# Performance work log

Measured on AMD Instinct MI355X. Metric: run time of the kernel, lower is better.

The kernel has to match this reference:

```python
import jax, jax.numpy as jnp
import numpy as np

N = 100000   # num nodes
E = 500000   # num hyperedges
NNZ = 1600000
H, C = 4, 32
IN_CH = 128


def setup_inputs() -> dict:
    key = jax.random.key(0)
    k1, k2, k3, k4, k5 = jax.random.split(key, 5)
    X = jax.random.normal(k1, (N, IN_CH), dtype=jnp.float32)
    W = jax.random.normal(k2, (IN_CH, H * C), dtype=jnp.float32) * (1.0 / np.sqrt(IN_CH))
    att_e = jax.random.normal(k3, (1, H, C), dtype=jnp.float32) * 0.1
    vertex = jax.random.randint(k4, (NNZ,), 0, N, dtype=jnp.int64)
    edges = jax.random.randint(k5, (NNZ,), 0, E, dtype=jnp.int64)
    return {"X": X, "W": W, "att_e": att_e, "vertex": vertex, "edges": edges}


def reference(X, W, att_e, vertex, edges):
    n = X.shape[0]
    X0 = X @ W                                  # [N, H*C]
    Xh = X0.reshape(n, H, C)                    # [N, H, C]
    Xve = Xh[vertex]                            # [nnz, H, C] gather
    # scatter-mean over hyperedges
    esum = jax.ops.segment_sum(Xve, edges, num_segments=E)            # [E, H, C]
    cnt = jax.ops.segment_sum(jnp.ones((Xve.shape[0],), X.dtype), edges, num_segments=E)
    Xe = esum / jnp.maximum(cnt, 1.0)[:, None, None]                  # [E, H, C]
    # per-edge attention score
    alpha_e = (Xe * att_e).sum(-1)              # [E, H]
    a_ev = alpha_e[edges]                       # [nnz, H]
    alpha = jax.nn.leaky_relu(a_ev, 0.01)
    # segment softmax over vertex groups
    m = jax.ops.segment_max(alpha, vertex, num_segments=n)            # [N, H]
    ex = jnp.exp(alpha - m[vertex])
    den = jax.ops.segment_sum(ex, vertex, num_segments=n)             # [N, H]
    alpha = ex / (den[vertex] + 1e-16)          # [nnz, H]
    # weighted scatter-sum back to nodes
    Xev = Xe[edges] * alpha[:, :, None]         # [nnz, H, C]
    Xv = jax.ops.segment_sum(Xev, vertex, num_segments=n)             # [N, H, C]
    return Xv.reshape(n, H * C) + X0
```

## Files before the change

### kernel.cpp

```cpp
#include <hip/hip_runtime.h>
#include <hip/hip_bf16.h>
#include <hip/hip_fp16.h>
#include <cstdint>

#define NH 4
#define HC 128
#define INCH 128
#define NEDGE 500000
#define NN 100000

#define KE_SHIFT 11
#define KV_SHIFT 9
#define KE (1 << KE_SHIFT)
#define KV (1 << KV_SHIFT)
#define NBE 245
#define NBV 196
#define CAP_E 8192
#define CAP_V 10240
#define CHUNK_A 4096

typedef float          f32x2 __attribute__((ext_vector_type(2)));
typedef float          f32x4 __attribute__((ext_vector_type(4)));
typedef float          f32x8 __attribute__((ext_vector_type(8)));
typedef unsigned int   u32x2 __attribute__((ext_vector_type(2)));
typedef unsigned short u16x8 __attribute__((ext_vector_type(8)));

static __device__ __forceinline__ unsigned short f2bf(float f){
  union { float f; unsigned u; } v; v.f = f;
  unsigned r = v.u + 0x7fffu + ((v.u >> 16) & 1u);
  return (unsigned short)(r >> 16);
}
static __device__ __forceinline__ float bf2f(unsigned short b){
  union { unsigned u; float f; } v; v.u = ((unsigned)b) << 16;
  return v.f;
}
static __device__ __forceinline__ f32x8 bf8f(u16x8 b){
  f32x8 r;
  r[0]=bf2f(b[0]); r[1]=bf2f(b[1]); r[2]=bf2f(b[2]); r[3]=bf2f(b[3]);
  r[4]=bf2f(b[4]); r[5]=bf2f(b[5]); r[6]=bf2f(b[6]); r[7]=bf2f(b[7]);
  return r;
}

#if __has_builtin(__builtin_amdgcn_cvt_pk_fp8_f32) && __has_builtin(__builtin_amdgcn_cvt_pk_f32_fp8)
#define FP8_HW 1
#else
#define FP8_HW 0
#endif

#if !FP8_HW
static __device__ __forceinline__ unsigned enc1_fp8(float v){
  union{ __half h; unsigned short u; } c; c.h = __float2half(v);
  unsigned u = c.u;
  unsigned s = (u>>15)&1u, e=(u>>10)&31u, m=u&0x3FFu;
  int e8 = (int)e - 8;
  unsigned lsb = (m>>7)&1u;
  unsigned m8 = (m + 63u + lsb) >> 7;
  if (m8 == 8u){ m8 = 0u; e8 += 1; }
  if (e8 <= 0)  return s<<7;
  if (e8 >= 16) return (s<<7)|0x7Eu;
  return (s<<7)|((unsigned)e8<<3)|m8;
}
static __device__ __forceinline__ float dec1_fp8(unsigned b){
  unsigned s=(b>>7)&1u, e=(b>>3)&15u, m=b&7u;
  union{unsigned u; float f;} r;
  if (e==0u){ r.f = (float)m * 0.001953125f; if(s) r.f = -r.f; }
  else r.u = (s<<31)|((e+120u)<<23)|(m<<20);
  return r.f;
}
#endif

static __device__ __forceinline__ u32x2 pack8_fp8(const f32x8 v){
  u32x2 w;
#if FP8_HW
  int w0 = __builtin_amdgcn_cvt_pk_fp8_f32(v[0], v[1], 0, false);
  w0     = __builtin_amdgcn_cvt_pk_fp8_f32(v[2], v[3], w0, true);
  int w1 = __builtin_amdgcn_cvt_pk_fp8_f32(v[4], v[5], 0, false);
  w1     = __builtin_amdgcn_cvt_pk_fp8_f32(v[6], v[7], w1, true);
  w.x = (unsigned)w0; w.y = (unsigned)w1;
#else
  w.x = enc1_fp8(v[0]) | (enc1_fp8(v[1])<<8) | (enc1_fp8(v[2])<<16) | (enc1_fp8(v[3])<<24);
  w.y = enc1_fp8(v[4]) | (enc1_fp8(v[5])<<8) | (enc1_fp8(v[6])<<16) | (enc1_fp8(v[7])<<24);
#endif
  return w;
}
static __device__ __forceinline__ void fma8s_fp8(f32x8& acc, float c, float w, u32x2 q){
#if FP8_HW
  f32x2 p;
  p = __builtin_amdgcn_cvt_pk_f32_fp8((int)q.x, false); acc[0]=acc[0]*c + w*p.x; acc[1]=acc[1]*c + w*p.y;
  p = __builtin_amdgcn_cvt_pk_f32_fp8((int)q.x, true ); acc[2]=acc[2]*c + w*p.x; acc[3]=acc[3]*c + w*p.y;
  p = __builtin_amdgcn_cvt_pk_f32_fp8((int)q.y, false); acc[4]=acc[4]*c + w*p.x; acc[5]=acc[5]*c + w*p.y;
  p = __builtin_amdgcn_cvt_pk_f32_fp8((int)q.y, true ); acc[6]=acc[6]*c + w*p.x; acc[7]=acc[7]*c + w*p.y;
#else
  acc[0]=acc[0]*c + w*dec1_fp8(q.x&0xFF);        acc[1]=acc[1]*c + w*dec1_fp8((q.x>>8)&0xFF);
  acc[2]=acc[2]*c + w*dec1_fp8((q.x>>16)&0xFF);  acc[3]=acc[3]*c + w*dec1_fp8(q.x>>24);
  acc[4]=acc[4]*c + w*dec1_fp8(q.y&0xFF);        acc[5]=acc[5]*c + w*dec1_fp8((q.y>>8)&0xFF);
  acc[6]=acc[6]*c + w*dec1_fp8((q.y>>16)&0xFF);  acc[7]=acc[7]*c + w*dec1_fp8(q.y>>24);
#endif
}

#define GBM 128
#define GBK 16
__global__ __launch_bounds__(256) void gemmA_fused(const float* __restrict__ X,
                                                   const float* __restrict__ Wm,
                                                   const float* __restrict__ att,
                                                   unsigned short* __restrict__ X0bf,
                                                   float* __restrict__ score, int nrows,
                                                   const int* __restrict__ vertex,
                                                   const int* __restrict__ edges, int nnz,
                                                   int* __restrict__ cursE, int* __restrict__ cursV,
                                                   unsigned* __restrict__ stgE, unsigned* __restrict__ stgV,
                                                   int nA){
  __shared__ float As[GBK][GBM+4];
  __shared__ float Bs[GBK][HC+4];
  __shared__ float sc[GBM][17];
  __shared__ int cE[NBE], c2E[NBE], gE[NBE];
  __shared__ int cV[NBV], c2V[NBV], gV[NBV];
  const int t = threadIdx.x;

  if ((int)blockIdx.x < nA){
    const int base = blockIdx.x * CHUNK_A;
    int ev[16], vv[16];
    #pragma unroll
    for (int j=0;j<16;j++){
      int i = base + t + j*256;
      if (i < nnz){ ev[j] = edges[i]; vv[j] = vertex[i]; }
      else ev[j] = -1;
    }
    for (int j=t;j<NBE;j+=256){ cE[j]=0; c2E[j]=0; }
    for (int j=t;j<NBV;j+=256){ cV[j]=0; c2V[j]=0; }
    __syncthreads();
    #pragma unroll
    for (int j=0;j<16;j++) if (ev[j]>=0){
      atomicAdd(&cE[ev[j]>>KE_SHIFT], 1);
      atomicAdd(&cV[vv[j]>>KV_SHIFT], 1);
    }
    __syncthreads();
    for (int j=t;j<NBE;j+=256) gE[j] = atomicAdd(&cursE[j], cE[j]);
    for (int j=t;j<NBV;j+=256) gV[j] = atomicAdd(&cursV[j], cV[j]);
    __syncthreads();
    #pragma unroll
    for (int j=0;j<16;j++) if (ev[j]>=0){
      int bE = ev[j]>>KE_SHIFT;
      int p = gE[bE] + atomicAdd(&c2E[bE],1);
      if (p < CAP_E) stgE[(size_t)bE*CAP_E + p] = ((unsigned)vv[j] << KE_SHIFT) | (unsigned)(ev[j] & (KE-1));
      int bV = vv[j]>>KV_SHIFT;
      int q = gV[bV] + atomicAdd(&c2V[bV],1);
      if (q < CAP_V) stgV[(size_t)bV*CAP_V + q] = ((unsigned)ev[j] << KV_SHIFT) | (unsigned)(vv[j] & (KV-1));
    }
    return;
  }

  const int row0 = (blockIdx.x - nA) * GBM;
  const int trow = t >> 4;
  const int tcol = t & 15;
  float acc[8][8];
  #pragma unroll
  for (int i=0;i<8;i++)
    #pragma unroll
    for (int j=0;j<8;j++) acc[i][j]=0.f;

  for (int k0=0;k0<INCH;k0+=GBK){
    #pragma unroll
    for (int l = t; l < 512; l += 256){
      int r  = l >> 2;
      int ks = (l & 3) * 4;
      int grow = row0 + r;
      float4 v = make_float4(0.f,0.f,0.f,0.f);
      if (grow < nrows) v = *(const float4*)(X + (size_t)grow*INCH + k0 + ks);
      As[ks+0][r]=v.x; As[ks+1][r]=v.y; As[ks+2][r]=v.z; As[ks+3][r]=v.w;
    }
    #pragma unroll
    for (int l = t; l < 512; l += 256){
      int r  = l >> 5;
      int cs = (l & 31) * 4;
      float4 v = *(const float4*)(Wm + (size_t)(k0+r)*HC + cs);
      *(float4*)(&Bs[r][cs]) = v;
    }
    __syncthreads();
    #pragma unroll
    for (int kk=0;kk<GBK;kk++){
      float a[8], b[8];
      *(float4*)&a[0] = *(float4*)&As[kk][trow*8];
      *(float4*)&a[4] = *(float4*)&As[kk][trow*8+4];
      *(float4*)&b[0] = *(float4*)&Bs[kk][tcol*8];
      *(float4*)&b[4] = *(float4*)&Bs[kk][tcol*8+4];
      #pragma unroll
      for (int i=0;i<8;i++)
        #pragma unroll
        for (int j=0;j<8;j++) acc[i][j] = fmaf(a[i], b[j], acc[i][j]);
    }
    __syncthreads();
  }
  float attv[8];
  *(float4*)&attv[0] = *(const float4*)(att + tcol*8);
  *(float4*)&attv[4] = *(const float4*)(att + tcol*8 + 4);
  #pragma unroll
  for (int i=0;i<8;i++){
    int grow = row0 + trow*8 + i;
    float p = 0.f;
    #pragma unroll
    for (int j=0;j<8;j++) p = fmaf(acc[i][j], attv[j], p);
    sc[trow*8+i][tcol] = p;
    if (grow < nrows){
      ushort4 b0, b1;
      b0.x=f2bf(acc[i][0]); b0.y=f2bf(acc[i][1]); b0.z=f2bf(acc[i][2]); b0.w=f2bf(acc[i][3]);
      b1.x=f2bf(acc[i][4]); b1.y=f2bf(acc[i][5]); b1.z=f2bf(acc[i][6]); b1.w=f2bf(acc[i][7]);
      *(ushort4*)(X0bf + (size_t)grow*HC + tcol*8    ) = b0;
      *(ushort4*)(X0bf + (size_t)grow*HC + tcol*8 + 4) = b1;
    }
  }
  __syncthreads();
  for (int idx = t; idx < GBM*NH; idx += 256){
    int row = idx >> 2, h = idx & 3;
    int grow = row0 + row;
    if (grow < nrows){
      float s = sc[row][4*h] + sc[row][4*h+1] + sc[row][4*h+2] + sc[row][4*h+3];
      score[(size_t)grow*NH + h] = s;
    }
  }
}

template<int K, int CAP, int IT, int SHIFT, int NB>
__device__ __forceinline__ void phaseB_body(const unsigned* __restrict__ stg,
                                            const int* __restrict__ curs,
                                            int* __restrict__ offsOut,
                                            int* __restrict__ csrOut, int nKeys, int b,
                                            int* cur, int* tsum, int* bsh){
  const int t = threadIdx.x;
  const int k0 = b * K;
  const int kc = min(K, nKeys - k0);
  int c = (t < NB) ? min(curs[t], CAP) : 0;
  bsh[t] = c; __syncthreads();
  for (int d2=1; d2<512; d2<<=1){
    int x = (t>=d2) ? bsh[t-d2] : 0; __syncthreads();
    bsh[t] += x; __syncthreads();
  }
  const int gbase = (b > 0) ? bsh[b-1] : 0;
  const int cnt   = min(curs[b], CAP);
  if (b == NB-1 && t == 0) offsOut[nKeys] = bsh[NB-1];
  unsigned it[IT];
  #pragma unroll
  for (int j=0;j<IT;j++){
    int i = t + j*512;
    it[j] = (i < cnt) ? stg[(size_t)b*CAP + i] : 0xFFFFFFFFu;
  }
  for (int j=t;j<K;j+=512) cur[j] = 0;
  __syncthreads();
  #pragma unroll
  for (int j=0;j<IT;j++) if (it[j] != 0xFFFFFFFFu) atomicAdd(&cur[it[j] & (K-1)], 1);
  __syncthreads();
  constexpr int KPT = K / 512;
  int loc[KPT]; int s = 0;
  #pragma unroll
  for (int j=0;j<KPT;j++){ loc[j] = s; s += cur[t*KPT + j]; }
  tsum[t] = s; __syncthreads();
  for (int d2=1; d2<512; d2<<=1){
    int x = (t>=d2) ? tsum[t-d2] : 0; __syncthreads();
    tsum[t] += x; __syncthreads();
  }
  const int tbase = tsum[t] - s;
  __syncthreads();
  #pragma unroll
  for (int j=0;j<KPT;j++){
    int k = t*KPT + j;
    int abs0 = gbase + tbase + loc[j];
    if (k < kc) offsOut[k0 + k] = abs0;
    cur[k] = abs0;
  }
  __syncthreads();
  #pragma unroll
  for (int j=0;j<IT;j++) if (it[j] != 0xFFFFFFFFu){
    int pos = atomicAdd(&cur[it[j] & (K-1)], 1);
    csrOut[pos] = (int)(it[j] >> SHIFT);
  }
}

__global__ __launch_bounds__(512) void phaseB_fused(const unsigned* __restrict__ stgE,
                                                    const unsigned* __restrict__ stgV,
                                                    const int* __restrict__ cursE,
                                                    const int* __restrict__ cursV,
                                                    int* __restrict__ eoffs, int* __restrict__ voffs,
                                                    int* __restrict__ ecsr, int* __restrict__ vcsr){
  __shared__ int cur[KE];
  __shared__ int tsum[512];
  __shared__ int bsh[512];
  const int b = blockIdx.x;
  if (b < NBE) phaseB_body<KE, CAP_E, CAP_E/512, KE_SHIFT, NBE>(stgE, cursE, eoffs, ecsr, NEDGE, b, cur, tsum, bsh);
  else         phaseB_body<KV, CAP_V, CAP_V/512, KV_SHIFT, NBV>(stgV, cursV, voffs, vcsr, NN, b - NBE, cur, tsum, bsh);
}

__global__ __launch_bounds__(256) void edge_agg(const unsigned short* __restrict__ X0bf,
                                                const float* __restrict__ score,
                                                const int* __restrict__ ecsr,
                                                const int* __restrict__ eoffs,
                                                unsigned char* __restrict__ Xe8,
                                                float* __restrict__ alphaS, int E){
  int eg = blockIdx.x * 16 + (threadIdx.x >> 4);
  if (eg >= E) return;
  const int lane  = threadIdx.x & 15;
  const int cbase = lane * 8;
  const int start = eoffs[eg];
  const int d     = eoffs[eg+1] - start;
  f32x8 acc0 = {0.f,0.f,0.f,0.f,0.f,0.f,0.f,0.f};
  f32x8 acc1 = {0.f,0.f,0.f,0.f,0.f,0.f,0.f,0.f};
  float sacc0 = 0.f, sacc1 = 0.f;
  int k = 0;
  for (; k+1<d; k+=2){
    int v0 = ecsr[start + k];
    int v1 = ecsr[start + k + 1];
    u16x8 x0 = *(const u16x8*)(X0bf + (size_t)v0*HC + cbase);
    u16x8 x1 = *(const u16x8*)(X0bf + (size_t)v1*HC + cbase);
    if (lane < NH){
      sacc0 += score[(size_t)v0*NH + lane];
      sacc1 += score[(size_t)v1*NH + lane];
    }
    acc0 += bf8f(x0);
    acc1 += bf8f(x1);
  }
  if (k < d){
    int v0 = ecsr[start + k];
    u16x8 x0 = *(const u16x8*)(X0bf + (size_t)v0*HC + cbase);
    if (lane < NH) sacc0 += score[(size_t)v0*NH + lane];
    acc0 += bf8f(x0);
  }
  acc0 += acc1;
  const float inv = 1.0f / fmaxf((float)d, 1.0f);
  acc0 *= inv;
  float lm = fmaxf(fmaxf(fmaxf(fabsf(acc0[0]),fabsf(acc0[1])),fmaxf(fabsf(acc0[2]),fabsf(acc0[3]))),
                   fmaxf(fmaxf(fabsf(acc0[4]),fabsf(acc0[5])),fmaxf(fabsf(acc0[6]),fabsf(acc0[7]))));
  #pragma unroll
  for (int s=1; s<16; s<<=1) lm = fmaxf(lm, __shfl_xor(lm, s, 16));
  const float qs  = (lm > 1e-30f) ? 448.0f/lm : 0.f;
  const float dqs = (lm > 1e-30f) ? lm*(1.0f/448.0f) : 0.f;
  f32x8 q = acc0 * qs;
  u32x2 w = pack8_fp8(q);
  *(u32x2*)(Xe8 + (size_t)eg*HC + cbase) = w;
  if (lane < NH){
    float a = (sacc0 + sacc1) * inv;
    a = a > 0.f ? a : 0.01f*a;
    f32x2 rec = { a, dqs };
    *(f32x2*)(alphaS + (size_t)eg*8 + lane*2) = rec;
  }
}

__global__ __launch_bounds__(256) void vert_pass(const unsigned short* __restrict__ X0bf,
                                                 const unsigned char* __restrict__ Xe8,
                                                 const float* __restrict__ alphaS,
                                                 const int* __restrict__ vcsr,
                                                 const int* __restrict__ voffs,
                                                 float* __restrict__ out, int N){
  int n = blockIdx.x * 16 + (threadIdx.x >> 4);
  if (n >= N) return;
  const int lane  = threadIdx.x & 15;
  const int cbase = lane * 8;
  const int h2    = (lane >> 2) * 2;
  const size_t obase = (size_t)n*HC + cbase;
  f32x8 x0 = bf8f(*(const u16x8*)(X0bf + obase));
  const int start = voffs[n];
  const int d     = voffs[n+1] - start;
  if (d == 0){
    f32x4 lo = {x0[0],x0[1],x0[2],x0[3]}, hi = {x0[4],x0[5],x0[6],x0[7]};
    __builtin_nontemporal_store(lo, (f32x4*)(out + obase));
    __builtin_nontemporal_store(hi, (f32x4*)(out + obase + 4));
    return;
  }

  float m0=-1e30f, m1=-1e30f, m2=-1e30f, m3=-1e30f;
  float den0=0.f, den1=0.f, den2=0.f, den3=0.f;
  f32x8 acc0 = {0.f,0.f,0.f,0.f,0.f,0.f,0.f,0.f};
  f32x8 acc1 = {0.f,0.f,0.f,0.f,0.f,0.f,0.f,0.f};
  f32x8 acc2 = {0.f,0.f,0.f,0.f,0.f,0.f,0.f,0.f};
  f32x8 acc3 = {0.f,0.f,0.f,0.f,0.f,0.f,0.f,0.f};

#define UPD(i, ar, q) { \
    float mn_ = fmaxf(m##i, (ar).x); \
    float c_  = __expf(m##i - mn_); \
    float p_  = __expf((ar).x - mn_); \
    den##i = den##i * c_ + p_; \
    fma8s_fp8(acc##i, c_, p_ * (ar).y, (q)); \
    m##i = mn_; }

  int k = 0;
  for (; k+3<d; k+=4){
    int e0 = vcsr[start + k];
    int e1 = vcsr[start + k + 1];
    int e2 = vcsr[start + k + 2];
    int e3 = vcsr[start + k + 3];
    f32x2 ar0 = *(const f32x2*)(alphaS + (size_t)e0*8 + h2);
    f32x2 ar1 = *(const f32x2*)(alphaS + (size_t)e1*8 + h2);
    f32x2 ar2 = *(const f32x2*)(alphaS + (size_t)e2*8 + h2);
    f32x2 ar3 = *(const f32x2*)(alphaS + (size_t)e3*8 + h2);
    u32x2 q0 = *(const u32x2*)(Xe8 + (size_t)e0*HC + cbase);
    u32x2 q1 = *(const u32x2*)(Xe8 + (size_t)e1*HC + cbase);
    u32x2 q2 = *(const u32x2*)(Xe8 + (size_t)e2*HC + cbase);
    u32x2 q3 = *(const u32x2*)(Xe8 + (size_t)e3*HC + cbase);
    UPD(0, ar0, q0);
    UPD(1, ar1, q1);
    UPD(2, ar2, q2);
    UPD(3, ar3, q3);
  }
  for (; k<d; k++){
    int e0 = vcsr[start + k];
    f32x2 ar0 = *(const f32x2*)(alphaS + (size_t)e0*8 + h2);
    u32x2 q0 = *(const u32x2*)(Xe8 + (size_t)e0*HC + cbase);
    UPD(0, ar0, q0);
  }
#undef UPD

  float mn = fmaxf(fmaxf(m0,m1), fmaxf(m2,m3));
  float c0 = __expf(m0-mn), c1 = __expf(m1-mn), c2 = __expf(m2-mn), c3 = __expf(m3-mn);
  float den = den0*c0 + den1*c1 + den2*c2 + den3*c3;
  f32x8 acc = acc0*c0 + acc1*c1 + acc2*c2 + acc3*c3;
  const float w = 1.0f / (den + 1e-16f);
  acc = acc*w + x0;
  f32x4 lo = {acc[0],acc[1],acc[2],acc[3]};
  f32x4 hi = {acc[4],acc[5],acc[6],acc[7]};
  __builtin_nontemporal_store(lo, (f32x4*)(out + obase));
  __builtin_nontemporal_store(hi, (f32x4*)(out + obase + 4));
}

extern "C" void kernel_launch(void* const* d_in, const int* in_sizes, int n_in,
                              void* d_out, int out_size, void* d_ws, size_t ws_size,
                              hipStream_t stream){
  const float* X   = (const float*)d_in[0];
  const float* Wm  = (const float*)d_in[1];
  const float* att = (const float*)d_in[2];
  const int* vertex = (const int*)d_in[3];
  const int* edges  = (const int*)d_in[4];
  const int N   = in_sizes[0] / INCH;
  const int NNZ = in_sizes[3];
  const int E   = NEDGE;

  char* ws = (char*)d_ws;
  size_t off = 0;
  auto alloc = [&](size_t bytes)->char*{
    char* p = ws + off;
    off += (bytes + 255) & ~(size_t)255;
    return p;
  };
  unsigned char*  Xe8    = (unsigned char*)alloc((size_t)E * HC);
  unsigned short* X0bf   = (unsigned short*)alloc((size_t)NN * HC * sizeof(unsigned short));
  float*          score  = (float*)alloc((size_t)NN * NH * sizeof(float));
  float*          alphaS = (float*)alloc((size_t)E * 8 * sizeof(float));
  int*            eoffs  = (int*)alloc((size_t)(E+1) * sizeof(int));
  int*            voffs  = (int*)alloc((size_t)(NN+1) * sizeof(int));
  int*            ecsr   = (int*)alloc((size_t)NNZ * sizeof(int));
  int*            vcsr   = (int*)alloc((size_t)NNZ * sizeof(int));
  int*            curs   = (int*)alloc((size_t)(NBE + NBV) * sizeof(int));
  int*            cursE  = curs;
  int*            cursV  = curs + NBE;
  unsigned* stgE = (unsigned*)(void*)Xe8;
  unsigned* stgV = (unsigned*)((char*)(void*)Xe8 + (size_t)NBE * CAP_E * sizeof(unsigned));

  const int nGemm = (N + GBM - 1) / GBM;
  const int nA    = (NNZ + CHUNK_A - 1) / CHUNK_A;

  hipMemsetAsync(curs, 0, (size_t)(NBE + NBV) * sizeof(int), stream);
  gemmA_fused<<<nA + nGemm, 256, 0, stream>>>(X, Wm, att, X0bf, score, N,
                                              vertex, edges, NNZ, cursE, cursV, stgE, stgV, nA);
  phaseB_fused<<<NBE + NBV, 512, 0, stream>>>(stgE, stgV, cursE, cursV, eoffs, voffs, ecsr, vcsr);
  edge_agg<<<(E + 15)/16, 256, 0, stream>>>(X0bf, score, ecsr, eoffs, Xe8, alphaS, E);
  vert_pass<<<(N + 15)/16, 256, 0, stream>>>(X0bf, Xe8, alphaS, vcsr, voffs, (float*)d_out, N);
}
```

Before: 256.8 us.

## Split fused GEMM/binning kernel, enlarge binning blocks, pack alpha records as fp16

Separates the combined GEMM and COO-binning kernel into two launches. Binning now runs in 512-thread blocks over 8192-element chunks, which halves the number of global cursor atomics. The per-edge alpha record shrinks from eight floats to a 16-byte record: four fp16 leaky-relu scores plus the fp32 dequant scale. vert_pass now issues one 16-byte load per edge instead of a strided f32x2 gather. The costs are an extra kernel launch, lost overlap between the GEMM and binning, and fp16 precision on the attention scores.

```diff
diff --git a/kernel.cpp b/kernel.cpp
--- a/kernel.cpp
+++ b/kernel.cpp
@@ -17,12 +17,13 @@
 #define NBV 196
 #define CAP_E 8192
 #define CAP_V 10240
-#define CHUNK_A 4096
+#define CHUNK_A 8192
 
 typedef float          f32x2 __attribute__((ext_vector_type(2)));
 typedef float          f32x4 __attribute__((ext_vector_type(4)));
 typedef float          f32x8 __attribute__((ext_vector_type(8)));
 typedef unsigned int   u32x2 __attribute__((ext_vector_type(2)));
+typedef unsigned int   u32x4 __attribute__((ext_vector_type(4)));
 typedef unsigned short u16x8 __attribute__((ext_vector_type(8)));
 
 static __device__ __forceinline__ unsigned short f2bf(float f){
@@ -100,59 +101,18 @@
 
 #define GBM 128
 #define GBK 16
-__global__ __launch_bounds__(256) void gemmA_fused(const float* __restrict__ X,
-                                                   const float* __restrict__ Wm,
-                                                   const float* __restrict__ att,
-                                                   unsigned short* __restrict__ X0bf,
-                                                   float* __restrict__ score, int nrows,
-                                                   const int* __restrict__ vertex,
-                                                   const int* __restrict__ edges, int nnz,
-                                                   int* __restrict__ cursE, int* __restrict__ cursV,
-                                                   unsigned* __restrict__ stgE, unsigned* __restrict__ stgV,
-                                                   int nA){
+__global__ __launch_bounds__(256) void gemm_x0(const float* __restrict__ X,
+                                               const float* __restrict__ Wm,
+                                               const float* __restrict__ att,
+                                               unsigned short* __restrict__ X0bf,
+                                               float* __restrict__ score, int nrows){
   __shared__ float As[GBK][GBM+4];
   __shared__ float Bs[GBK][HC+4];
   __shared__ float sc[GBM][17];
-  __shared__ int cE[NBE], c2E[NBE], gE[NBE];
-  __shared__ int cV[NBV], c2V[NBV], gV[NBV];
-  const int t = threadIdx.x;
-
-  if ((int)blockIdx.x < nA){
-    const int base = blockIdx.x * CHUNK_A;
-    int ev[16], vv[16];
-    #pragma unroll
-    for (int j=0;j<16;j++){
-      int i = base + t + j*256;
-      if (i < nnz){ ev[j] = edges[i]; vv[j] = vertex[i]; }
-      else ev[j] = -1;
-    }
-    for (int j=t;j<NBE;j+=256){ cE[j]=0; c2E[j]=0; }
-    for (int j=t;j<NBV;j+=256){ cV[j]=0; c2V[j]=0; }
-    __syncthreads();
-    #pragma unroll
-    for (int j=0;j<16;j++) if (ev[j]>=0){
-      atomicAdd(&cE[ev[j]>>KE_SHIFT], 1);
-      atomicAdd(&cV[vv[j]>>KV_SHIFT], 1);
-    }
-    __syncthreads();
-    for (int j=t;j<NBE;j+=256) gE[j] = atomicAdd(&cursE[j], cE[j]);
-    for (int j=t;j<NBV;j+=256) gV[j] = atomicAdd(&cursV[j], cV[j]);
-    __syncthreads();
-    #pragma unroll
-    for (int j=0;j<16;j++) if (ev[j]>=0){
-      int bE = ev[j]>>KE_SHIFT;
-      int p = gE[bE] + atomicAdd(&c2E[bE],1);
-      if (p < CAP_E) stgE[(size_t)bE*CAP_E + p] = ((unsigned)vv[j] << KE_SHIFT) | (unsigned)(ev[j] & (KE-1));
-      int bV = vv[j]>>KV_SHIFT;
-      int q = gV[bV] + atomicAdd(&c2V[bV],1);
-      if (q < CAP_V) stgV[(size_t)bV*CAP_V + q] = ((unsigned)ev[j] << KV_SHIFT) | (unsigned)(vv[j] & (KV-1));
-    }
-    return;
-  }
-
-  const int row0 = (blockIdx.x - nA) * GBM;
-  const int trow = t >> 4;
-  const int tcol = t & 15;
+  const int tid  = threadIdx.x;
+  const int row0 = blockIdx.x * GBM;
+  const int trow = tid >> 4;
+  const int tcol = tid & 15;
   float acc[8][8];
   #pragma unroll
   for (int i=0;i<8;i++)
@@ -161,7 +121,7 @@
 
   for (int k0=0;k0<INCH;k0+=GBK){
     #pragma unroll
-    for (int l = t; l < 512; l += 256){
+    for (int l = tid; l < 512; l += 256){
       int r  = l >> 2;
       int ks = (l & 3) * 4;
       int grow = row0 + r;
@@ -170,7 +130,7 @@
       As[ks+0][r]=v.x; As[ks+1][r]=v.y; As[ks+2][r]=v.z; As[ks+3][r]=v.w;
     }
     #pragma unroll
-    for (int l = t; l < 512; l += 256){
+    for (int l = tid; l < 512; l += 256){
       int r  = l >> 5;
       int cs = (l & 31) * 4;
       float4 v = *(const float4*)(Wm + (size_t)(k0+r)*HC + cs);
@@ -210,13 +170,51 @@
     }
   }
   __syncthreads();
-  for (int idx = t; idx < GBM*NH; idx += 256){
+  for (int idx = tid; idx < GBM*NH; idx += 256){
     int row = idx >> 2, h = idx & 3;
     int grow = row0 + row;
     if (grow < nrows){
       float s = sc[row][4*h] + sc[row][4*h+1] + sc[row][4*h+2] + sc[row][4*h+3];
       score[(size_t)grow*NH + h] = s;
     }
+  }
+}
+
+__global__ __launch_bounds__(512) void phaseA(const int* __restrict__ vertex,
+                                              const int* __restrict__ edges, int nnz,
+                                              int* __restrict__ cursE, int* __restrict__ cursV,
+                                              unsigned* __restrict__ stgE, unsigned* __restrict__ stgV){
+  __shared__ int cE[NBE], c2E[NBE], gE[NBE];
+  __shared__ int cV[NBV], c2V[NBV], gV[NBV];
+  const int t = threadIdx.x;
+  const int base = blockIdx.x * CHUNK_A;
+  int ev[16], vv[16];
+  #pragma unroll
+  for (int j=0;j<16;j++){
+    int i = base + t + j*512;
+    if (i < nnz){ ev[j] = edges[i]; vv[j] = vertex[i]; }
+    else ev[j] = -1;
+  }
+  for (int j=t;j<NBE;j+=512){ cE[j]=0; c2E[j]=0; }
+  for (int j=t;j<NBV;j+=512){ cV[j]=0; c2V[j]=0; }
+  __syncthreads();
+  #pragma unroll
+  for (int j=0;j<16;j++) if (ev[j]>=0){
+    atomicAdd(&cE[ev[j]>>KE_SHIFT], 1);
+    atomicAdd(&cV[vv[j]>>KV_SHIFT], 1);
+  }
+  __syncthreads();
+  for (int j=t;j<NBE;j+=512) gE[j] = atomicAdd(&cursE[j], cE[j]);
+  for (int j=t;j<NBV;j+=512) gV[j] = atomicAdd(&cursV[j], cV[j]);
+  __syncthreads();
+  #pragma unroll
+  for (int j=0;j<16;j++) if (ev[j]>=0){
+    int bE = ev[j]>>KE_SHIFT;
+    int p = gE[bE] + atomicAdd(&c2E[bE],1);
+    if (p < CAP_E) stgE[(size_t)bE*CAP_E + p] = ((unsigned)vv[j] << KE_SHIFT) | (unsigned)(ev[j] & (KE-1));
+    int bV = vv[j]>>KV_SHIFT;
+    int q = gV[bV] + atomicAdd(&c2V[bV],1);
+    if (q < CAP_V) stgV[(size_t)bV*CAP_V + q] = ((unsigned)ev[j] << KV_SHIFT) | (unsigned)(vv[j] & (KV-1));
   }
 }
 
@@ -294,7 +292,7 @@
                                                 const int* __restrict__ ecsr,
                                                 const int* __restrict__ eoffs,
                                                 unsigned char* __restrict__ Xe8,
-                                                float* __restrict__ alphaS, int E){
+                                                unsigned* __restrict__ alphaS, int E){
   int eg = blockIdx.x * 16 + (threadIdx.x >> 4);
   if (eg >= E) return;
   const int lane  = threadIdx.x & 15;
@@ -335,17 +333,25 @@
   f32x8 q = acc0 * qs;
   u32x2 w = pack8_fp8(q);
   *(u32x2*)(Xe8 + (size_t)eg*HC + cbase) = w;
-  if (lane < NH){
-    float a = (sacc0 + sacc1) * inv;
-    a = a > 0.f ? a : 0.01f*a;
-    f32x2 rec = { a, dqs };
-    *(f32x2*)(alphaS + (size_t)eg*8 + lane*2) = rec;
+  float aa = (sacc0 + sacc1) * inv;
+  aa = aa > 0.f ? aa : 0.01f*aa;
+  float a0 = __shfl(aa, 0, 16);
+  float a1 = __shfl(aa, 1, 16);
+  float a2 = __shfl(aa, 2, 16);
+  float a3 = __shfl(aa, 3, 16);
+  if (lane == 0){
+    u32x4 rec;
+    rec.x = (unsigned)__half_as_ushort(__float2half(a0)) | ((unsigned)__half_as_ushort(__float2half(a1)) << 16);
+    rec.y = (unsigned)__half_as_ushort(__float2half(a2)) | ((unsigned)__half_as_ushort(__float2half(a3)) << 16);
+    rec.z = __float_as_uint(dqs);
+    rec.w = 0u;
+    *(u32x4*)(alphaS + (size_t)eg*4) = rec;
   }
 }
 
 __global__ __launch_bounds__(256) void vert_pass(const unsigned short* __restrict__ X0bf,
                                                  const unsigned char* __restrict__ Xe8,
-                                                 const float* __restrict__ alphaS,
+                                                 const unsigned* __restrict__ alphaS,
                                                  const int* __restrict__ vcsr,
                                                  const int* __restrict__ voffs,
                                                  float* __restrict__ out, int N){
@@ -353,7 +359,7 @@
   if (n >= N) return;
   const int lane  = threadIdx.x & 15;
   const int cbase = lane * 8;
-  const int h2    = (lane >> 2) * 2;
+  const int h     = lane >> 2;
   const size_t obase = (size_t)n*HC + cbase;
   f32x8 x0 = bf8f(*(const u16x8*)(X0bf + obase));
   const int start = voffs[n];
@@ -372,12 +378,19 @@
   f32x8 acc2 = {0.f,0.f,0.f,0.f,0.f,0.f,0.f,0.f};
   f32x8 acc3 = {0.f,0.f,0.f,0.f,0.f,0.f,0.f,0.f};
 
-#define UPD(i, ar, q) { \
-    float mn_ = fmaxf(m##i, (ar).x); \
+#define EXTRACT(rec, aval, sval) { \
+    unsigned word_ = (h < 2) ? (rec).x : (rec).y; \
+    unsigned h16_  = (h & 1) ? (word_ >> 16) : (word_ & 0xFFFFu); \
+    aval = __half2float(__ushort_as_half((unsigned short)h16_)); \
+    sval = __uint_as_float((rec).z); }
+
+#define UPD(i, rec, q) { \
+    float a_, s_; EXTRACT(rec, a_, s_); \
+    float mn_ = fmaxf(m##i, a_); \
     float c_  = __expf(m##i - mn_); \
-    float p_  = __expf((ar).x - mn_); \
+    float p_  = __expf(a_ - mn_); \
     den##i = den##i * c_ + p_; \
-    fma8s_fp8(acc##i, c_, p_ * (ar).y, (q)); \
+    fma8s_fp8(acc##i, c_, p_ * s_, (q)); \
     m##i = mn_; }
 
   int k = 0;
@@ -386,26 +399,27 @@
     int e1 = vcsr[start + k + 1];
     int e2 = vcsr[start + k + 2];
     int e3 = vcsr[start + k + 3];
-    f32x2 ar0 = *(const f32x2*)(alphaS + (size_t)e0*8 + h2);
-    f32x2 ar1 = *(const f32x2*)(alphaS + (size_t)e1*8 + h2);
-    f32x2 ar2 = *(const f32x2*)(alphaS + (size_t)e2*8 + h2);
-    f32x2 ar3 = *(const f32x2*)(alphaS + (size_t)e3*8 + h2);
+    u32x4 r0 = *(const u32x4*)(alphaS + (size_t)e0*4);
+    u32x4 r1 = *(const u32x4*)(alphaS + (size_t)e1*4);
+    u32x4 r2 = *(const u32x4*)(alphaS + (size_t)e2*4);
+    u32x4 r3 = *(const u32x4*)(alphaS + (size_t)e3*4);
     u32x2 q0 = *(const u32x2*)(Xe8 + (size_t)e0*HC + cbase);
     u32x2 q1 = *(const u32x2*)(Xe8 + (size_t)e1*HC + cbase);
     u32x2 q2 = *(const u32x2*)(Xe8 + (size_t)e2*HC + cbase);
     u32x2 q3 = *(const u32x2*)(Xe8 + (size_t)e3*HC + cbase);
-    UPD(0, ar0, q0);
-    UPD(1, ar1, q1);
-    UPD(2, ar2, q2);
-    UPD(3, ar3, q3);
+    UPD(0, r0, q0);
+    UPD(1, r1, q1);
+    UPD(2, r2, q2);
+    UPD(3, r3, q3);
   }
   for (; k<d; k++){
     int e0 = vcsr[start + k];
-    f32x2 ar0 = *(const f32x2*)(alphaS + (size_t)e0*8 + h2);
+    u32x4 r0 = *(const u32x4*)(alphaS + (size_t)e0*4);
     u32x2 q0 = *(const u32x2*)(Xe8 + (size_t)e0*HC + cbase);
-    UPD(0, ar0, q0);
+    UPD(0, r0, q0);
   }
 #undef UPD
+#undef EXTRACT
 
   float mn = fmaxf(fmaxf(m0,m1), fmaxf(m2,m3));
   float c0 = __expf(m0-mn), c1 = __expf(m1-mn), c2 = __expf(m2-mn), c3 = __expf(m3-mn);
@@ -441,7 +455,7 @@
   unsigned char*  Xe8    = (unsigned char*)alloc((size_t)E * HC);
   unsigned short* X0bf   = (unsigned short*)alloc((size_t)NN * HC * sizeof(unsigned short));
   float*          score  = (float*)alloc((size_t)NN * NH * sizeof(float));
-  float*          alphaS = (float*)alloc((size_t)E * 8 * sizeof(float));
+  unsigned*       alphaS = (unsigned*)alloc((size_t)E * 4 * sizeof(unsigned));
   int*            eoffs  = (int*)alloc((size_t)(E+1) * sizeof(int));
   int*            voffs  = (int*)alloc((size_t)(NN+1) * sizeof(int));
   int*            ecsr   = (int*)alloc((size_t)NNZ * sizeof(int));
@@ -452,12 +466,9 @@
   unsigned* stgE = (unsigned*)(void*)Xe8;
   unsigned* stgV = (unsigned*)((char*)(void*)Xe8 + (size_t)NBE * CAP_E * sizeof(unsigned));
 
-  const int nGemm = (N + GBM - 1) / GBM;
-  const int nA    = (NNZ + CHUNK_A - 1) / CHUNK_A;
-
   hipMemsetAsync(curs, 0, (size_t)(NBE + NBV) * sizeof(int), stream);
-  gemmA_fused<<<nA + nGemm, 256, 0, stream>>>(X, Wm, att, X0bf, score, N,
-                                              vertex, edges, NNZ, cursE, cursV, stgE, stgV, nA);
+  gemm_x0<<<(N + GBM - 1)/GBM, 256, 0, stream>>>(X, Wm, att, X0bf, score, N);
+  phaseA<<<(NNZ + CHUNK_A - 1)/CHUNK_A, 512, 0, stream>>>(vertex, edges, NNZ, cursE, cursV, stgE, stgV);
   phaseB_fused<<<NBE + NBV, 512, 0, stream>>>(stgE, stgV, cursE, cursV, eoffs, voffs, ecsr, vcsr);
   edge_agg<<<(E + 15)/16, 256, 0, stream>>>(X0bf, score, ecsr, eoffs, Xe8, alphaS, E);
   vert_pass<<<(N + 15)/16, 256, 0, stream>>>(X0bf, Xe8, alphaS, vcsr, voffs, (float*)d_out, N);
```

Result: no change. 260.6 us (+1.5%).
